# Performance work log

Measured on AMD Instinct MI355X. Metric: run time of the kernel, lower is better.

The kernel has to match this reference:

```python
import jax, jax.numpy as jnp
import numpy as np

N, E, G = 50000, 1600000, 512
IN, HID, PROJ = 128, 128, 256


def setup_inputs() -> dict:
    key = jax.random.key(0)
    ks = jax.random.split(key, 20)
    s = 0.05
    return {
        'x1': jax.random.normal(ks[0], (N, IN), jnp.float32),
        'edge_index1': jax.random.randint(ks[1], (2, E), 0, N),
        'batch1': jnp.sort(jax.random.randint(ks[2], (N,), 0, G)),
        'x2': jax.random.normal(ks[3], (N, IN), jnp.float32),
        'edge_index2': jax.random.randint(ks[4], (2, E), 0, N),
        'batch2': jnp.sort(jax.random.randint(ks[5], (N,), 0, G)),
        'W1': jax.random.normal(ks[6], (IN, HID), jnp.float32) * s,
        'b1': jnp.zeros((HID,), jnp.float32),
        'W2': jax.random.normal(ks[7], (HID, HID), jnp.float32) * s,
        'b2': jnp.zeros((HID,), jnp.float32),
        'W3': jax.random.normal(ks[8], (HID, HID), jnp.float32) * s,
        'b3': jnp.zeros((HID,), jnp.float32),
        'Wp1': jax.random.normal(ks[9], (HID, PROJ), jnp.float32) * s,
        'bp1': jnp.zeros((PROJ,), jnp.float32),
        'gamma1': jnp.ones((PROJ,), jnp.float32),
        'beta1': jnp.zeros((PROJ,), jnp.float32),
        'Wp2': jax.random.normal(ks[10], (PROJ, PROJ), jnp.float32) * s,
        'bp2': jnp.zeros((PROJ,), jnp.float32),
        'gamma2': jnp.ones((PROJ,), jnp.float32),
        'beta2': jnp.zeros((PROJ,), jnp.float32),
        'Wq1': jax.random.normal(ks[11], (PROJ, PROJ // 2), jnp.float32) * s,
        'bq1': jnp.zeros((PROJ // 2,), jnp.float32),
        'Wq2': jax.random.normal(ks[12], (PROJ // 2, PROJ), jnp.float32) * s,
        'bq2': jnp.zeros((PROJ,), jnp.float32),
    }


def _gcn_conv(x, src, dst, W, b):
    # PyG GCNConv: add self-loops, symmetric norm, gather -> scatter-add
    n = x.shape[0]
    h = x @ W                                   # [n, out]
    loop = jnp.arange(n)
    s = jnp.concatenate([src, loop])
    d = jnp.concatenate([dst, loop])
    deg = jax.ops.segment_sum(jnp.ones(s.shape[0], h.dtype), d, num_segments=n)
    dinv = jnp.where(deg > 0, 1.0 / jnp.sqrt(deg), 0.0)
    norm = (dinv[s] * dinv[d])[:, None]         # [E+n, 1]
    out = jax.ops.segment_sum(h[s] * norm, d, num_segments=n)
    return out + b


def _encode(x, edge_index, batch, W1, b1, W2, b2, W3, b3):
    src, dst = edge_index[0], edge_index[1]
    h = jax.nn.relu(_gcn_conv(x, src, dst, W1, b1))
    h = jax.nn.relu(_gcn_conv(h, src, dst, W2, b2)) + h
    h = jax.nn.relu(_gcn_conv(h, src, dst, W3, b3)) + h
    # global mean pool over graph ids
    s = jax.ops.segment_sum(h, batch, num_segments=G)
    cnt = jax.ops.segment_sum(jnp.ones(h.shape[0], h.dtype), batch, num_segments=G)
    return s / jnp.maximum(cnt, 1.0)[:, None]


def _batchnorm(x, gamma, beta):
    m = x.mean(axis=0)
    v = x.var(axis=0)  # biased, matches torch BN normalization
    return gamma * (x - m) / jnp.sqrt(v + 1e-5) + beta


def _projector(h, Wp1, bp1, g1, be1, Wp2, bp2, g2, be2):
    z = jax.nn.relu(_batchnorm(h @ Wp1 + bp1, g1, be1))
    return _batchnorm(z @ Wp2 + bp2, g2, be2)


def _predictor(z, Wq1, bq1, Wq2, bq2):
    return jax.nn.relu(z @ Wq1 + bq1) @ Wq2 + bq2


def reference(x1, edge_index1, batch1, x2, edge_index2, batch2,
              W1, b1, W2, b2, W3, b3,
              Wp1, bp1, gamma1, beta1, Wp2, bp2, gamma2, beta2,
              Wq1, bq1, Wq2, bq2):
    h1 = _encode(x1, edge_index1, batch1, W1, b1, W2, b2, W3, b3)
    h2 = _encode(x2, edge_index2, batch2, W1, b1, W2, b2, W3, b3)
    z1 = _projector(h1, Wp1, bp1, gamma1, beta1, Wp2, bp2, gamma2, beta2)
    z2 = _projector(h2, Wp1, bp1, gamma1, beta1, Wp2, bp2, gamma2, beta2)
    p1 = _predictor(z1, Wq1, bq1, Wq2, bq2)
    p2 = _predictor(z2, Wq1, bq1, Wq2, bq2)
    return (p1, p2, z1, z2)
```

## Files before the change

### kernel.cpp

```cpp
#include <hip/hip_runtime.h>
#include <hip/hip_bf16.h>

#define NN     50000
#define NN2    100000
#define NEDGE  1600000
#define NE2    3200000
#define NG     512
#define FIN    128
#define FHID   128
#define FPROJ  256

#define BSH    9
#define BSZ    512
#define NBUCK  98
#define NBUCK2 196
#define EPB    8192
#define NABLK  196
#define NABLK2 392
#define NHIST2 (NBUCK2*NABLK2)
#define NSB1   ((NHIST2 + 255) / 256)

#define SRCSH  12
#define NKEY   (BSZ * 16)

typedef __attribute__((ext_vector_type(8))) short short8;
typedef __attribute__((ext_vector_type(4))) float f32x4;
typedef __attribute__((ext_vector_type(2))) float f32x2;

static __device__ __forceinline__ short f2bf(float f) {
    union { float f; unsigned u; } x; x.f = f;
    unsigned r = (x.u + 0x7FFFu + ((x.u >> 16) & 1u)) >> 16;
    return (short)(r & 0xFFFFu);
}
static __device__ __forceinline__ float bf2f(unsigned short u) {
    union { unsigned u; float f; } x; x.u = ((unsigned)u) << 16;
    return x.f;
}
static __device__ __forceinline__ float bflo(unsigned u) {
    union { unsigned u; float f; } x; x.u = u << 16; return x.f;
}
static __device__ __forceinline__ float bfhi(unsigned u) {
    union { unsigned u; float f; } x; x.u = u & 0xFFFF0000u; return x.f;
}
static __device__ __forceinline__ unsigned packbf(float a, float b) {
    return (unsigned)(unsigned short)f2bf(a) | ((unsigned)(unsigned short)f2bf(b) << 16);
}
static __device__ __forceinline__ f32x2 bfpair(unsigned u) {
    union { unsigned v[2]; f32x2 f; } x;
    x.v[0] = u << 16;
    x.v[1] = u & 0xFFFF0000u;
    return x.f;
}


__global__ __launch_bounds__(1024) void k_bhist(const int* __restrict__ dst0,
                                                const int* __restrict__ dst1,
                                                int* __restrict__ histG,
                                                unsigned short* __restrict__ lrank) {
    __shared__ int h[NBUCK2];
    for (int j = threadIdx.x; j < NBUCK2; j += 1024) h[j] = 0;
    __syncthreads();
    int b = blockIdx.x;
    int g = b / NABLK, blk = b % NABLK;
    const int* dst = g ? dst1 : dst0;
    int base = blk * EPB;
    int gb = g * NBUCK;
    for (int t = threadIdx.x; t < EPB; t += 1024) {
        int i = base + t;
        if (i < NEDGE)
            lrank[(size_t)g * NEDGE + i] =
                (unsigned short)atomicAdd(&h[gb + (dst[i] >> BSH)], 1);
    }
    __syncthreads();
    for (int j = threadIdx.x; j < NBUCK2; j += 1024)
        histG[(size_t)j * NABLK2 + b] = h[j];
}

__global__ void s_scan256(const int* __restrict__ in, int* __restrict__ out,
                          int* __restrict__ bsum, int n) {
    __shared__ int s[256];
    int i = blockIdx.x * 256 + threadIdx.x;
    int v = (i < n) ? in[i] : 0;
    s[threadIdx.x] = v;
    for (int o = 1; o < 256; o <<= 1) {
        __syncthreads();
        int t = (threadIdx.x >= o) ? s[threadIdx.x - o] : 0;
        __syncthreads();
        s[threadIdx.x] += t;
    }
    __syncthreads();
    if (i < n) out[i] = s[threadIdx.x] - v;
    if (threadIdx.x == 255) bsum[blockIdx.x] = s[255];
}

__global__ __launch_bounds__(512) void s_scan_tail(int* __restrict__ bsum, int nb) {
    __shared__ int s[512];
    int v = (threadIdx.x < nb) ? bsum[threadIdx.x] : 0;
    s[threadIdx.x] = v;
    for (int o = 1; o < 512; o <<= 1) {
        __syncthreads();
        int t = (threadIdx.x >= o) ? s[threadIdx.x - o] : 0;
        __syncthreads();
        s[threadIdx.x] += t;
    }
    __syncthreads();
    if (threadIdx.x < nb) bsum[threadIdx.x] = s[threadIdx.x] - v;
}

__global__ void s_add(int* __restrict__ out, const int* __restrict__ bs, int n) {
    int i = blockIdx.x * 256 + threadIdx.x;
    if (i < n) out[i] += bs[blockIdx.x];
}

__global__ __launch_bounds__(1024) void k_part(const int* __restrict__ src0,
                                               const int* __restrict__ dst0,
                                               const int* __restrict__ src1,
                                               const int* __restrict__ dst1,
                                               const unsigned short* __restrict__ lrank,
                                               const int* __restrict__ histS,
                                               unsigned* __restrict__ pedge) {
    int b = blockIdx.x;
    int g = b / NABLK, blk = b % NABLK;
    const int* src = g ? src1 : src0;
    const int* dst = g ? dst1 : dst0;
    int base = blk * EPB;
    int gb = g * NBUCK;
    for (int t = threadIdx.x; t < EPB; t += 1024) {
        int i = base + t;
        if (i < NEDGE) {
            int d = dst[i];
            int pos = histS[(size_t)(gb + (d >> BSH)) * NABLK2 + b]
                      + (int)lrank[(size_t)g * NEDGE + i];
            pedge[pos] = (unsigned)src[i] | ((unsigned)(d & (BSZ - 1)) << 16);
        }
    }
}

__global__ __launch_bounds__(256) void k_csr(const unsigned* __restrict__ pedge,
                                             const int* __restrict__ histS,
                                             int* __restrict__ csroff,
                                             unsigned short* __restrict__ csrc,
                                             float* __restrict__ dinv) {
    __shared__ int cnt[NKEY];
    __shared__ int part[256];
    int k = blockIdx.x;
    int g = k / NBUCK;
    int nl0 = (k - g * NBUCK) * BSZ;
    int beg = histS[(size_t)k * NABLK2];
    int end = (k == NBUCK2 - 1) ? NE2 : histS[(size_t)(k + 1) * NABLK2];
    int t = threadIdx.x;
    for (int j = t; j < NKEY; j += 256) cnt[j] = 0;
    __syncthreads();
    for (int e = beg + t; e < end; e += 256) {
        unsigned v = pedge[e];
        int key = (int)((v >> 16) << 4) | (int)((v & 0xFFFFu) >> SRCSH);
        atomicAdd(&cnt[key], 1);
    }
    __syncthreads();
    int base = t * 32;
    int s = 0;
#pragma unroll
    for (int j = 0; j < 32; ++j) s += cnt[base + j];
    part[t] = s;
    for (int o = 1; o < 256; o <<= 1) {
        __syncthreads();
        int v2 = (t >= o) ? part[t - o] : 0;
        __syncthreads();
        part[t] += v2;
    }
    __syncthreads();
    int run = part[t] - s;
#pragma unroll
    for (int j = 0; j < 32; ++j) { int c = cnt[base + j]; cnt[base + j] = run; run += c; }
    __syncthreads();
    for (int tt = t; tt < BSZ; tt += 256) {
        int nl = nl0 + tt;
        if (nl < NN) {
            int gn = g * NN + nl;
            int d0 = cnt[tt * 16];
            int d1 = (tt == BSZ - 1) ? (end - beg) : cnt[(tt + 1) * 16];
            csroff[gn] = beg + d0;
            dinv[gn] = 1.0f / sqrtf((float)(d1 - d0 + 1));
        }
    }
    __syncthreads();
    for (int e = beg + t; e < end; e += 256) {
        unsigned v = pedge[e];
        int key = (int)((v >> 16) << 4) | (int)((v & 0xFFFFu) >> SRCSH);
        int r = atomicAdd(&cnt[key], 1);
        csrc[beg + r] = (unsigned short)(v & 0xFFFFu);
    }
    if (k == NBUCK2 - 1 && t == 0) csroff[NN2] = NE2;
}


__global__ void k_prepw(const float* __restrict__ W0, const float* __restrict__ W1,
                        const float* __restrict__ W2, short* __restrict__ Wf) {
    int b = blockIdx.x;
    int l = b >> 5; b &= 31;
    const float* W = (l == 0) ? W0 : (l == 1) ? W1 : W2;
    int nt = b >> 2, kt = b & 3;
    int lane = threadIdx.x;
    int n = nt * 16 + (lane & 15);
    int kbase = kt * 32 + (lane >> 4) * 8;
    short8 v;
#pragma unroll
    for (int j = 0; j < 8; ++j) v[j] = f2bf(W[(kbase + j) * FHID + n]);
    *(short8*)(Wf + (size_t)l * 16384 + (size_t)((nt * 4 + kt) * 64 + lane) * 8) = v;
}

__global__ __launch_bounds__(256) void k_gemm(const float* __restrict__ x1,
                                              const float* __restrict__ x2,
                                              const unsigned short* __restrict__ Abf,
                                              const short* __restrict__ Wf,
                                              const float* __restrict__ dinv,
                                              unsigned short* __restrict__ hp) {
    int lane = threadIdx.x & 63;
    int wv = threadIdx.x >> 6;
    int quad = lane >> 4;
    int rowbase = blockIdx.x * 64 + wv * 16;
    int arow = rowbase + (lane & 15);
    if (arow >= NN2) arow = NN2 - 1;

    f32x4 acc[8];
#pragma unroll
    for (int i = 0; i < 8; ++i) acc[i] = (f32x4){0.f, 0.f, 0.f, 0.f};

#pragma unroll
    for (int kt = 0; kt < 4; ++kt) {
        short8 af;
        if (Abf) {
            af = *(const short8*)(Abf + (size_t)arow * FIN + kt * 32 + quad * 8);
        } else {
            const float* ap = (arow < NN ? x1 + (size_t)arow * FIN
                                         : x2 + (size_t)(arow - NN) * FIN)
                              + kt * 32 + quad * 8;
            float4 a0 = *(const float4*)ap;
            float4 a1 = *(const float4*)(ap + 4);
            af[0] = f2bf(a0.x); af[1] = f2bf(a0.y); af[2] = f2bf(a0.z); af[3] = f2bf(a0.w);
            af[4] = f2bf(a1.x); af[5] = f2bf(a1.y); af[6] = f2bf(a1.z); af[7] = f2bf(a1.w);
        }
#pragma unroll
        for (int nt = 0; nt < 8; ++nt) {
            short8 bf = *(const short8*)(Wf + (size_t)((nt * 4 + kt) * 64 + lane) * 8);
            acc[nt] = __builtin_amdgcn_mfma_f32_16x16x32_bf16(af, bf, acc[nt], 0, 0, 0);
        }
    }
    float4 dv = *(const float4*)(dinv + rowbase + quad * 4);
    float dvv[4] = {dv.x, dv.y, dv.z, dv.w};
    int col = lane & 15;
#pragma unroll
    for (int r = 0; r < 4; ++r) {
        int orow = rowbase + quad * 4 + r;
        if (orow < NN2) {
#pragma unroll
            for (int nt = 0; nt < 8; ++nt)
                hp[(size_t)orow * FHID + nt * 16 + col] =
                    (unsigned short)f2bf(acc[nt][r] * dvv[r]);
        }
    }
}


#define LDI(S, EE) { _Pragma("unroll") for (int j = 0; j < 8; ++j) S[j] = (int)csrc[(EE) + j]; }
#define GTH(V, S)  { _Pragma("unroll") for (int j = 0; j < 8; ++j) V[j] = hpg[(size_t)S[j] * 16 + l16]; }
#define ACC8(V)    { _Pragma("unroll") for (int j = 0; j < 8; ++j) { \
                       a0 += bfpair(V[j].x); a1 += bfpair(V[j].y);   \
                       a2 += bfpair(V[j].z); a3 += bfpair(V[j].w); } }

__global__ __launch_bounds__(256) void k_agg(const uint4* __restrict__ hp4,
                                             const int* __restrict__ off,
                                             const unsigned short* __restrict__ csrc,
                                             const float* __restrict__ dinv,
                                             const float* __restrict__ bias,
                                             const unsigned short* __restrict__ resid,
                                             unsigned short* __restrict__ hout) {
    int tid = threadIdx.x;
    int l16 = tid & 15;
    int grp = tid >> 4;
    int gn = blockIdx.x * 16 + grp;
    int g = gn >= NN;
    int node = gn - g * NN;
    const uint4* hpg = hp4 + (size_t)g * NN * 16;
    int beg = off[gn], end = off[gn + 1];

    uint4 sv = hpg[(size_t)node * 16 + l16];
    f32x2 a0 = bfpair(sv.x), a1 = bfpair(sv.y), a2 = bfpair(sv.z), a3 = bfpair(sv.w);

    int nb = (end - beg) >> 3;
    int e = beg + (nb << 3);
    if (nb >= 2) {
        int s0[8], s1[8];
        uint4 v0[8], v1[8];
        int ee = beg;
        LDI(s0, ee);
        GTH(v0, s0);
        LDI(s1, ee + 8);
        ee += 16;
        int k = 1;
        while (k + 2 <= nb) {
            GTH(v1, s1);
            LDI(s0, ee); ee += 8;
            ACC8(v0);
            GTH(v0, s0);
            LDI(s1, ee); ee += 8;
            ACC8(v1);
            k += 2;
        }
        if (k < nb) {
            GTH(v1, s1);
            ACC8(v0);
            ACC8(v1);
        } else {
            ACC8(v0);
        }
    } else if (nb == 1) {
        int s0[8]; uint4 v0[8];
        LDI(s0, beg);
        GTH(v0, s0);
        ACC8(v0);
    }
    for (; e + 2 <= end; e += 2) {
        int t0 = (int)csrc[e], t1 = (int)csrc[e + 1];
        uint4 w0 = hpg[(size_t)t0 * 16 + l16];
        uint4 w1 = hpg[(size_t)t1 * 16 + l16];
        a0 += bfpair(w0.x); a1 += bfpair(w0.y); a2 += bfpair(w0.z); a3 += bfpair(w0.w);
        a0 += bfpair(w1.x); a1 += bfpair(w1.y); a2 += bfpair(w1.z); a3 += bfpair(w1.w);
    }
    for (; e < end; ++e) {
        uint4 w = hpg[(size_t)csrc[e] * 16 + l16];
        a0 += bfpair(w.x); a1 += bfpair(w.y); a2 += bfpair(w.z); a3 += bfpair(w.w);
    }

    float dv = dinv[gn];
    float4 b0 = ((const float4*)bias)[l16 * 2];
    float4 b1 = ((const float4*)bias)[l16 * 2 + 1];
    float o0 = fmaxf(a0.x * dv + b0.x, 0.f);
    float o1 = fmaxf(a0.y * dv + b0.y, 0.f);
    float o2 = fmaxf(a1.x * dv + b0.z, 0.f);
    float o3 = fmaxf(a1.y * dv + b0.w, 0.f);
    float o4 = fmaxf(a2.x * dv + b1.x, 0.f);
    float o5 = fmaxf(a2.y * dv + b1.y, 0.f);
    float o6 = fmaxf(a3.x * dv + b1.z, 0.f);
    float o7 = fmaxf(a3.y * dv + b1.w, 0.f);
    if (resid) {
        uint4 rv = ((const uint4*)resid)[(size_t)gn * 16 + l16];
        o0 += bflo(rv.x); o1 += bfhi(rv.x);
        o2 += bflo(rv.y); o3 += bfhi(rv.y);
        o4 += bflo(rv.z); o5 += bfhi(rv.z);
        o6 += bflo(rv.w); o7 += bfhi(rv.w);
    }
    uint4 ov;
    ov.x = packbf(o0, o1);
    ov.y = packbf(o2, o3);
    ov.z = packbf(o4, o5);
    ov.w = packbf(o6, o7);
    ((uint4*)hout)[(size_t)gn * 16 + l16] = ov;
}


static __device__ __forceinline__ int lbound(const int* __restrict__ a, int key) {
    int lo = 0, hi = NN;
    while (lo < hi) { int mid = (lo + hi) >> 1; if (a[mid] < key) lo = mid + 1; else hi = mid; }
    return lo;
}

__global__ void k_pool(const unsigned short* __restrict__ h,
                       const int* __restrict__ b0, const int* __restrict__ b1,
                       float* __restrict__ pooled, float* __restrict__ stats) {
    int b = blockIdx.x;
    int g = b >> 9, lg = b & 511;
    int c = threadIdx.x;
    if (b == 0) {
        for (int i = c; i < 2048; i += 128) stats[i] = 0.f;
    }
    const int* batch = g ? b1 : b0;
    int beg = lbound(batch, lg);
    int end = lbound(batch, lg + 1);
    const unsigned short* hb = h + (size_t)g * NN * FHID;
    float s = 0.f;
    for (int i = beg; i < end; ++i) s += bf2f(hb[(size_t)i * FHID + c]);
    int cnt = end - beg;
    pooled[(size_t)b * FHID + c] = s / (float)(cnt > 0 ? cnt : 1);
}


__global__ void k_mlp(const float* __restrict__ A, const float* __restrict__ W,
                      const float* __restrict__ bias, float* __restrict__ out,
                      int K, int Nc, int act,
                      float* __restrict__ statsOut,
                      const float* __restrict__ statsIn,
                      const float* __restrict__ gIn, const float* __restrict__ beIn) {
    __shared__ float As[8 * 256];
    __shared__ float scl[256], shf[256];
    int n = threadIdx.x;
    int r0 = blockIdx.x * 8;
    int g = blockIdx.x >> 6;
    if (statsIn && n < K) {
        const float* si = statsIn + g * 512;
        float m = si[n] * (1.f / 512.f);
        float var = si[K + n] * (1.f / 512.f) - m * m;
        float inv = 1.0f / sqrtf(var + 1e-5f);
        float s = gIn[n] * inv;
        scl[n] = s;
        shf[n] = beIn[n] - m * s;
    }
    __syncthreads();
    for (int idx = n; idx < 8 * K; idx += blockDim.x) {
        float v = A[(size_t)r0 * K + idx];
        if (statsIn) {
            int k = idx & (K - 1);
            v = fmaxf(v * scl[k] + shf[k], 0.f);
        }
        As[idx] = v;
    }
    __syncthreads();
    float bb = bias[n];
    float acc[8];
#pragma unroll
    for (int r = 0; r < 8; ++r) acc[r] = bb;
    for (int k = 0; k < K; ++k) {
        float w = W[(size_t)k * Nc + n];
#pragma unroll
        for (int r = 0; r < 8; ++r) acc[r] = fmaf(As[r * K + k], w, acc[r]);
    }
    if (statsOut) {
        float s = 0.f, q = 0.f;
#pragma unroll
        for (int r = 0; r < 8; ++r) { s += acc[r]; q += acc[r] * acc[r]; }
        atomicAdd(&statsOut[g * 512 + n], s);
        atomicAdd(&statsOut[g * 512 + Nc + n], q);
    }
#pragma unroll
    for (int r = 0; r < 8; ++r) {
        float v = acc[r];
        if (act) v = fmaxf(v, 0.f);
        out[(size_t)(r0 + r) * Nc + n] = v;
    }
}

__global__ void k_bnapply(const float* __restrict__ X, const float* __restrict__ stats,
                          const float* __restrict__ gamma, const float* __restrict__ beta,
                          float* __restrict__ out, int Nc, int act) {
    int i = blockIdx.x * 256 + threadIdx.x;
    if (i >= 1024 * Nc) return;
    int c = i % Nc;
    int g = i / (512 * Nc);
    const float* st = stats + g * 512;
    float m = st[c] * (1.f / 512.f);
    float var = st[Nc + c] * (1.f / 512.f) - m * m;
    float inv = 1.0f / sqrtf(var + 1e-5f);
    float v = gamma[c] * (X[i] - m) * inv + beta[c];
    if (act) v = fmaxf(v, 0.f);
    out[i] = v;
}


extern "C" void kernel_launch(void* const* d_in, const int* in_sizes, int n_in,
                              void* d_out, int out_size, void* d_ws, size_t ws_size,
                              hipStream_t stream) {
    const float* x1 = (const float*)d_in[0];
    const float* x2 = (const float*)d_in[3];
    const int*   ei[2]    = {(const int*)d_in[1], (const int*)d_in[4]};
    const int*   batch[2] = {(const int*)d_in[2], (const int*)d_in[5]};
    const float* W[3]  = {(const float*)d_in[6], (const float*)d_in[8], (const float*)d_in[10]};
    const float* bb[3] = {(const float*)d_in[7], (const float*)d_in[9], (const float*)d_in[11]};
    const float* Wp1 = (const float*)d_in[12]; const float* bp1 = (const float*)d_in[13];
    const float* g1  = (const float*)d_in[14]; const float* be1 = (const float*)d_in[15];
    const float* Wp2 = (const float*)d_in[16]; const float* bp2 = (const float*)d_in[17];
    const float* g2  = (const float*)d_in[18]; const float* be2 = (const float*)d_in[19];
    const float* Wq1 = (const float*)d_in[20]; const float* bq1 = (const float*)d_in[21];
    const float* Wq2 = (const float*)d_in[22]; const float* bq2 = (const float*)d_in[23];

    char* ws = (char*)d_ws;
    size_t off = 0;
    auto alloc = [&](size_t bytes) -> void* {
        void* p = ws + off;
        off += (bytes + 255) & ~(size_t)255;
        return p;
    };
    unsigned short* h_cur  = (unsigned short*)alloc((size_t)NN2 * FHID * 2);
    unsigned short* hp     = (unsigned short*)alloc((size_t)NN2 * FHID * 2);
    unsigned short* csrc   = (unsigned short*)alloc((size_t)(NE2 + 16) * 2);
    int*            csroff = (int*)alloc((size_t)(NN2 + 1) * 4);
    unsigned short* lrank  = (unsigned short*)alloc((size_t)NE2 * 2);
    unsigned*       pedge  = (unsigned*)alloc((size_t)NE2 * 4);
    int*            histG  = (int*)alloc((size_t)NHIST2 * 4);
    int*            histS  = (int*)alloc((size_t)NHIST2 * 4);
    int*            bsum   = (int*)alloc(512 * 4);
    float*          dinv   = (float*)alloc((size_t)100352 * 4);
    float*          pooled = (float*)alloc((size_t)2 * NG * FHID * 4);
    short*          Wf     = (short*)alloc((size_t)3 * 16384 * 2);
    float*          t1     = (float*)alloc((size_t)1024 * 256 * 4);
    float*          t2     = (float*)alloc((size_t)1024 * 256 * 4);
    float*          t3     = (float*)alloc((size_t)1024 * 128 * 4);
    float*          stats  = (float*)alloc(2048 * 4);

    const int* src0 = ei[0];           const int* dst0 = ei[0] + NEDGE;
    const int* src1 = ei[1];           const int* dst1 = ei[1] + NEDGE;

    k_prepw<<<96, 64, 0, stream>>>(W[0], W[1], W[2], Wf);

    k_bhist<<<NABLK2, 1024, 0, stream>>>(dst0, dst1, histG, lrank);
    s_scan256<<<NSB1, 256, 0, stream>>>(histG, histS, bsum, NHIST2);
    s_scan_tail<<<1, 512, 0, stream>>>(bsum, NSB1);
    s_add<<<NSB1, 256, 0, stream>>>(histS, bsum, NHIST2);
    k_part<<<NABLK2, 1024, 0, stream>>>(src0, dst0, src1, dst1, lrank, histS, pedge);
    k_csr<<<NBUCK2, 256, 0, stream>>>(pedge, histS, csroff, csrc, dinv);

    for (int l = 0; l < 3; ++l) {
        const unsigned short* Abf = (l == 0) ? nullptr : h_cur;
        const unsigned short* resid = (l == 0) ? nullptr : h_cur;
        k_gemm<<<1564, 256, 0, stream>>>(x1, x2, Abf, Wf + (size_t)l * 16384, dinv, hp);
        k_agg<<<6250, 256, 0, stream>>>((const uint4*)hp, csroff, csrc, dinv,
                                        bb[l], resid, h_cur);
    }
    k_pool<<<1024, 128, 0, stream>>>(h_cur, batch[0], batch[1], pooled, stats);

    float* outp = (float*)d_out;
    float* p_out = outp;
    float* z_out = outp + (size_t)2 * NG * FPROJ;
    float* st1 = stats, *st2 = stats + 1024;
    k_mlp<<<128, 256, 0, stream>>>(pooled, Wp1, bp1, t1,
                                   128, 256, 0, st1, nullptr, nullptr, nullptr);
    k_mlp<<<128, 256, 0, stream>>>(t1, Wp2, bp2, t2,
                                   256, 256, 0, st2, st1, g1, be1);
    k_bnapply<<<1024, 256, 0, stream>>>(t2, st2, g2, be2, z_out, 256, 0);
    k_mlp<<<128, 128, 0, stream>>>(z_out, Wq1, bq1, t3,
                                   256, 128, 1, nullptr, nullptr, nullptr, nullptr);
    k_mlp<<<128, 256, 0, stream>>>(t3, Wq2, bq2, p_out,
                                   128, 256, 0, nullptr, nullptr, nullptr, nullptr);
}
```

Measured before the change: 719.6 us.

## Stage per-block CSR indices in LDS for aggregation; widen CSR build to 512 threads

The aggregation kernel now first loads each block's contiguous neighbour-index range from global memory into shared memory, then reads gather indices from LDS. It also adds scheduling barriers to keep gathers batched and an occupancy hint in the launch bounds. The CSR build kernel moves from 256 to 512 threads so each thread handles one node. The LDS buffer is capped at 2048 edges per 16-node block with no fallback, so an unusually dense block would read stale indices; the self-loop term is also now added last, which changes summation order.

```diff
diff --git a/kernel.cpp b/kernel.cpp
--- a/kernel.cpp
+++ b/kernel.cpp
@@ -22,6 +22,8 @@
 
 #define SRCSH  12
 #define NKEY   (BSZ * 16)
+
+#define MAXE_BLK 2048
 
 typedef __attribute__((ext_vector_type(8))) short short8;
 typedef __attribute__((ext_vector_type(4))) float f32x4;
@@ -136,33 +138,33 @@
     }
 }
 
-__global__ __launch_bounds__(256) void k_csr(const unsigned* __restrict__ pedge,
+__global__ __launch_bounds__(512) void k_csr(const unsigned* __restrict__ pedge,
                                              const int* __restrict__ histS,
                                              int* __restrict__ csroff,
                                              unsigned short* __restrict__ csrc,
                                              float* __restrict__ dinv) {
     __shared__ int cnt[NKEY];
-    __shared__ int part[256];
+    __shared__ int part[512];
     int k = blockIdx.x;
     int g = k / NBUCK;
     int nl0 = (k - g * NBUCK) * BSZ;
     int beg = histS[(size_t)k * NABLK2];
     int end = (k == NBUCK2 - 1) ? NE2 : histS[(size_t)(k + 1) * NABLK2];
     int t = threadIdx.x;
-    for (int j = t; j < NKEY; j += 256) cnt[j] = 0;
-    __syncthreads();
-    for (int e = beg + t; e < end; e += 256) {
+    for (int j = t; j < NKEY; j += 512) cnt[j] = 0;
+    __syncthreads();
+    for (int e = beg + t; e < end; e += 512) {
         unsigned v = pedge[e];
         int key = (int)((v >> 16) << 4) | (int)((v & 0xFFFFu) >> SRCSH);
         atomicAdd(&cnt[key], 1);
     }
     __syncthreads();
-    int base = t * 32;
+    int base = t * 16;
     int s = 0;
 #pragma unroll
-    for (int j = 0; j < 32; ++j) s += cnt[base + j];
+    for (int j = 0; j < 16; ++j) s += cnt[base + j];
     part[t] = s;
-    for (int o = 1; o < 256; o <<= 1) {
+    for (int o = 1; o < 512; o <<= 1) {
         __syncthreads();
         int v2 = (t >= o) ? part[t - o] : 0;
         __syncthreads();
@@ -171,20 +173,20 @@
     __syncthreads();
     int run = part[t] - s;
 #pragma unroll
-    for (int j = 0; j < 32; ++j) { int c = cnt[base + j]; cnt[base + j] = run; run += c; }
-    __syncthreads();
-    for (int tt = t; tt < BSZ; tt += 256) {
-        int nl = nl0 + tt;
+    for (int j = 0; j < 16; ++j) { int c = cnt[base + j]; cnt[base + j] = run; run += c; }
+    __syncthreads();
+    {
+        int nl = nl0 + t;
         if (nl < NN) {
             int gn = g * NN + nl;
-            int d0 = cnt[tt * 16];
-            int d1 = (tt == BSZ - 1) ? (end - beg) : cnt[(tt + 1) * 16];
+            int d0 = cnt[t * 16];
+            int d1 = (t == BSZ - 1) ? (end - beg) : cnt[(t + 1) * 16];
             csroff[gn] = beg + d0;
             dinv[gn] = 1.0f / sqrtf((float)(d1 - d0 + 1));
         }
     }
     __syncthreads();
-    for (int e = beg + t; e < end; e += 256) {
+    for (int e = beg + t; e < end; e += 512) {
         unsigned v = pedge[e];
         int key = (int)((v >> 16) << 4) | (int)((v & 0xFFFFu) >> SRCSH);
         int r = atomicAdd(&cnt[key], 1);
@@ -262,75 +264,81 @@
 }
 
 
-#define LDI(S, EE) { _Pragma("unroll") for (int j = 0; j < 8; ++j) S[j] = (int)csrc[(EE) + j]; }
+#define SCHB __builtin_amdgcn_sched_barrier(0)
+#define RDI(S, EE) { _Pragma("unroll") for (int j = 0; j < 8; ++j) S[j] = (int)sidx[(EE) + j]; }
 #define GTH(V, S)  { _Pragma("unroll") for (int j = 0; j < 8; ++j) V[j] = hpg[(size_t)S[j] * 16 + l16]; }
 #define ACC8(V)    { _Pragma("unroll") for (int j = 0; j < 8; ++j) { \
                        a0 += bfpair(V[j].x); a1 += bfpair(V[j].y);   \
                        a2 += bfpair(V[j].z); a3 += bfpair(V[j].w); } }
 
-__global__ __launch_bounds__(256) void k_agg(const uint4* __restrict__ hp4,
-                                             const int* __restrict__ off,
-                                             const unsigned short* __restrict__ csrc,
-                                             const float* __restrict__ dinv,
-                                             const float* __restrict__ bias,
-                                             const unsigned short* __restrict__ resid,
-                                             unsigned short* __restrict__ hout) {
+__global__ __launch_bounds__(256, 4) void k_agg(const uint4* __restrict__ hp4,
+                                                const int* __restrict__ off,
+                                                const unsigned short* __restrict__ csrc,
+                                                const float* __restrict__ dinv,
+                                                const float* __restrict__ bias,
+                                                const unsigned short* __restrict__ resid,
+                                                unsigned short* __restrict__ hout) {
+    __shared__ unsigned short sidx[MAXE_BLK + 16];
     int tid = threadIdx.x;
     int l16 = tid & 15;
     int grp = tid >> 4;
-    int gn = blockIdx.x * 16 + grp;
+    int gnb = blockIdx.x * 16;
+    int blkBeg = off[gnb];
+    int blkLen = off[gnb + 16] - blkBeg;
+    if (blkLen > MAXE_BLK) blkLen = MAXE_BLK;
+    for (int i = tid; i < blkLen; i += 256)
+        sidx[i] = csrc[blkBeg + i];
+    __syncthreads();
+
+    int gn = gnb + grp;
     int g = gn >= NN;
     int node = gn - g * NN;
     const uint4* hpg = hp4 + (size_t)g * NN * 16;
     int beg = off[gn], end = off[gn + 1];
+    int lbeg = beg - blkBeg;
 
     uint4 sv = hpg[(size_t)node * 16 + l16];
-    f32x2 a0 = bfpair(sv.x), a1 = bfpair(sv.y), a2 = bfpair(sv.z), a3 = bfpair(sv.w);
-
-    int nb = (end - beg) >> 3;
-    int e = beg + (nb << 3);
-    if (nb >= 2) {
+    f32x2 a0 = (f32x2){0.f, 0.f}, a1 = (f32x2){0.f, 0.f};
+    f32x2 a2 = (f32x2){0.f, 0.f}, a3 = (f32x2){0.f, 0.f};
+
+    int n8 = (end - beg) >> 3;
+    if (n8 >= 2) {
         int s0[8], s1[8];
         uint4 v0[8], v1[8];
-        int ee = beg;
-        LDI(s0, ee);
-        GTH(v0, s0);
-        LDI(s1, ee + 8);
-        ee += 16;
+        int e = lbeg;
+        RDI(s0, e);
+        RDI(s1, e + 8);
+        GTH(v0, s0); SCHB;
+        e += 16;
         int k = 1;
-        while (k + 2 <= nb) {
-            GTH(v1, s1);
-            LDI(s0, ee); ee += 8;
+        while (k + 2 <= n8) {
+            GTH(v1, s1); SCHB;
+            RDI(s0, e); e += 8;
             ACC8(v0);
-            GTH(v0, s0);
-            LDI(s1, ee); ee += 8;
+            GTH(v0, s0); SCHB;
+            RDI(s1, e); e += 8;
             ACC8(v1);
             k += 2;
         }
-        if (k < nb) {
-            GTH(v1, s1);
+        if (k < n8) {
+            GTH(v1, s1); SCHB;
             ACC8(v0);
             ACC8(v1);
         } else {
             ACC8(v0);
         }
-    } else if (nb == 1) {
+    } else if (n8 == 1) {
         int s0[8]; uint4 v0[8];
-        LDI(s0, beg);
+        RDI(s0, lbeg);
         GTH(v0, s0);
         ACC8(v0);
     }
-    for (; e + 2 <= end; e += 2) {
-        int t0 = (int)csrc[e], t1 = (int)csrc[e + 1];
-        uint4 w0 = hpg[(size_t)t0 * 16 + l16];
-        uint4 w1 = hpg[(size_t)t1 * 16 + l16];
-        a0 += bfpair(w0.x); a1 += bfpair(w0.y); a2 += bfpair(w0.z); a3 += bfpair(w0.w);
-        a0 += bfpair(w1.x); a1 += bfpair(w1.y); a2 += bfpair(w1.z); a3 += bfpair(w1.w);
-    }
-    for (; e < end; ++e) {
-        uint4 w = hpg[(size_t)csrc[e] * 16 + l16];
+    int et = lbeg + (n8 << 3), lend = lbeg + (end - beg);
+    for (; et < lend; ++et) {
+        uint4 w = hpg[(size_t)sidx[et] * 16 + l16];
         a0 += bfpair(w.x); a1 += bfpair(w.y); a2 += bfpair(w.z); a3 += bfpair(w.w);
     }
+    a0 += bfpair(sv.x); a1 += bfpair(sv.y); a2 += bfpair(sv.z); a3 += bfpair(sv.w);
 
     float dv = dinv[gn];
     float4 b0 = ((const float4*)bias)[l16 * 2];
@@ -506,7 +514,7 @@
     s_scan_tail<<<1, 512, 0, stream>>>(bsum, NSB1);
     s_add<<<NSB1, 256, 0, stream>>>(histS, bsum, NHIST2);
     k_part<<<NABLK2, 1024, 0, stream>>>(src0, dst0, src1, dst1, lrank, histS, pedge);
-    k_csr<<<NBUCK2, 256, 0, stream>>>(pedge, histS, csroff, csrc, dinv);
+    k_csr<<<NBUCK2, 512, 0, stream>>>(pedge, histS, csroff, csrc, dinv);
 
     for (int l = 0; l < 3; ++l) {
         const unsigned short* Abf = (l == 0) ? nullptr : h_cur;
```

Result: slower. 916.7 us (+27.4%).
